# Performance work log

Measured on AMD Instinct MI355X. Metric: run time of the kernel, lower is better.

The kernel has to match this reference:

```python
import jax, jax.numpy as jnp
import numpy as np

N_HEADS = 8
KEY_DIM = 16
VALUE_DIM = 16
EMBED = N_HEADS * KEY_DIM  # 128
B, N = 32, 16384


def setup_inputs() -> dict:
    key = jax.random.key(0)
    k1, k2, k3, k4 = jax.random.split(key, 4)
    query = jax.random.normal(k1, (B, 1, EMBED), dtype=jnp.float32)
    keys = jax.random.normal(k2, (B, 1, N, EMBED), dtype=jnp.float32)
    values = jax.random.normal(k3, (B, 1, N, EMBED), dtype=jnp.float32)
    mask = jnp.zeros((B, 1, N), dtype=jnp.float32)  # additive mask
    W_out = jax.random.normal(k4, (N_HEADS * VALUE_DIM, EMBED), dtype=jnp.float32) * 0.05
    return {"query": query, "keys": keys, "values": values, "mask": mask, "W_out": W_out}


def _make_heads(v, d):
    # [B, N, H*d] -> [H, B, N, d]
    b, n, _ = v.shape
    return jnp.transpose(v.reshape(b, n, N_HEADS, d), (2, 0, 1, 3))


def reference(query, keys, values, mask, W_out):
    k = keys[:, 0]    # [B, N, E]
    v = values[:, 0]  # [B, N, E]
    q = _make_heads(query, KEY_DIM)   # [H, B, 1, dk]
    K = _make_heads(k, KEY_DIM)       # [H, B, N, dk]
    V = _make_heads(v, VALUE_DIM)     # [H, B, N, dv]
    scale = jnp.float32(KEY_DIM) ** 0.5
    attn = jnp.einsum('hbqd,hbnd->hbqn', q, K) / scale  # [H, B, 1, N]
    attn = attn + mask                                   # broadcast [B,1,N]
    attn = jax.nn.softmax(attn, axis=-1)
    heads = jnp.einsum('hbqn,hbnd->hbqd', attn, V)       # [H, B, 1, dv]
    b = heads.shape[1]
    concat = jnp.transpose(heads, (1, 2, 0, 3)).reshape(b, 1, N_HEADS * VALUE_DIM)
    return concat @ W_out  # [B, 1, E]
```

## Files before the change

kernel.cpp:

```cpp
#include <hip/hip_runtime.h>
#include <math.h>

#define NHEADS 8
#define KD 16
#define EMBED 128
#define BATCH 32
#define NSEQ 16384
#define NCHUNK 64
#define CHUNK (NSEQ / NCHUNK)
#define PART_STRIDE 18

typedef float f32x2 __attribute__((ext_vector_type(2)));

__global__ __launch_bounds__(256) void attn_partial(
    const float* __restrict__ q,
    const float* __restrict__ K,
    const float* __restrict__ V,
    const float* __restrict__ mask,
    float* __restrict__ part)
{
    const int b    = blockIdx.x >> 6;
    const int c    = blockIdx.x & 63;
    const int wave = threadIdx.x >> 6;
    const int lane = threadIdx.x & 63;
    const int head = lane >> 3;
    const int g    = lane & 7;

    const f32x2 q2 = *(const f32x2*)&q[b * EMBED + 2 * lane];

    float m = -INFINITY;
    float lsum = 0.f;
    float accx = 0.f, accy = 0.f;

    const size_t rowbase = (size_t)b * NSEQ;
    const int r0 = c * CHUNK;

    #pragma unroll 4
    for (int r = r0 + wave; r < r0 + CHUNK; r += 4) {
        const size_t off = (rowbase + r) * EMBED + 2 * lane;
        const f32x2 k2 = __builtin_nontemporal_load((const f32x2*)&K[off]);
        const f32x2 v2 = __builtin_nontemporal_load((const f32x2*)&V[off]);
        float p = q2.x * k2.x + q2.y * k2.y;
        p += __shfl_xor(p, 1);
        p += __shfl_xor(p, 2);
        p += __shfl_xor(p, 4);
        const float s  = p * 0.25f + mask[rowbase + r];
        const float mn = fmaxf(m, s);
        const float corr = __expf(m - mn);
        const float w    = __expf(s - mn);
        lsum = lsum * corr + w;
        accx = accx * corr + w * v2.x;
        accy = accy * corr + w * v2.y;
        m = mn;
    }

    __shared__ float lds[4][NHEADS][PART_STRIDE];
    lds[wave][head][2 + 2 * g]     = accx;
    lds[wave][head][2 + 2 * g + 1] = accy;
    if (g == 0) {
        lds[wave][head][0] = m;
        lds[wave][head][1] = lsum;
    }
    __syncthreads();

    const int t = threadIdx.x;
    if (t < EMBED) {
        const int h = t >> 4;
        const int d = t & 15;
        float M = -INFINITY;
        #pragma unroll
        for (int w = 0; w < 4; ++w) M = fmaxf(M, lds[w][h][0]);
        float L = 0.f, A = 0.f;
        #pragma unroll
        for (int w = 0; w < 4; ++w) {
            const float e = __expf(lds[w][h][0] - M);
            L += lds[w][h][1] * e;
            A += lds[w][h][2 + d] * e;
        }
        float* p = &part[((size_t)(b * NCHUNK + c) * NHEADS + h) * PART_STRIDE];
        p[2 + d] = A;
        if (d == 0) { p[0] = M; p[1] = L; }
    }
}

__global__ __launch_bounds__(128) void attn_finish(
    const float* __restrict__ part,
    const float* __restrict__ Wout,
    float* __restrict__ out)
{
    const int b = blockIdx.x;
    const int t = threadIdx.x;
    const int h = t >> 4;
    const int d = t & 15;

    __shared__ float heads[EMBED];

    float Mc[4], Lc[4], Ac[4];
    #pragma unroll
    for (int j = 0; j < 4; ++j) { Mc[j] = -INFINITY; Lc[j] = 0.f; Ac[j] = 0.f; }

    #pragma unroll 4
    for (int i = 0; i < 16; ++i) {
        #pragma unroll
        for (int j = 0; j < 4; ++j) {
            const int c = j * 16 + i;
            const float* p = &part[((size_t)(b * NCHUNK + c) * NHEADS + h) * PART_STRIDE];
            const float mc = p[0];
            const float lc = p[1];
            const float ac = p[2 + d];
            const float Mn = fmaxf(Mc[j], mc);
            const float eM = __expf(Mc[j] - Mn);
            const float ec = __expf(mc - Mn);
            Lc[j] = Lc[j] * eM + lc * ec;
            Ac[j] = Ac[j] * eM + ac * ec;
            Mc[j] = Mn;
        }
    }

    const float M = fmaxf(fmaxf(Mc[0], Mc[1]), fmaxf(Mc[2], Mc[3]));
    float L = 0.f, A = 0.f;
    #pragma unroll
    for (int j = 0; j < 4; ++j) {
        const float e = __expf(Mc[j] - M);
        L += Lc[j] * e;
        A += Ac[j] * e;
    }
    heads[t] = A / L;
    __syncthreads();

    float o = 0.f;
    #pragma unroll 8
    for (int dd = 0; dd < EMBED; ++dd)
        o += heads[dd] * Wout[dd * EMBED + t];
    out[b * EMBED + t] = o;
}

extern "C" void kernel_launch(void* const* d_in, const int* in_sizes, int n_in,
                              void* d_out, int out_size, void* d_ws, size_t ws_size,
                              hipStream_t stream) {
    const float* q    = (const float*)d_in[0];
    const float* K    = (const float*)d_in[1];
    const float* V    = (const float*)d_in[2];
    const float* mask = (const float*)d_in[3];
    const float* Wout = (const float*)d_in[4];
    float* out  = (float*)d_out;
    float* part = (float*)d_ws;

    attn_partial<<<BATCH * NCHUNK, 256, 0, stream>>>(q, K, V, mask, part);
    attn_finish<<<BATCH, 128, 0, stream>>>(part, Wout, out);
}
```

Measured before the change: 89.77 us.

## Fuse partial and finish kernels with last-block atomic counter reduction

Merges the two launches into one kernel. Each block writes its partial softmax state, then increments a per-batch atomic counter, and the last block for each batch does the cross-chunk merge and the output projection. This removes the second kernel launch and its dependency gap. In exchange it adds a memset launch to reset the counters, plus fences and an atomic per block.

```diff
diff --git a/kernel.cpp b/kernel.cpp
--- a/kernel.cpp
+++ b/kernel.cpp
@@ -9,15 +9,19 @@
 #define NCHUNK 64
 #define CHUNK (NSEQ / NCHUNK)
 #define PART_STRIDE 18
+#define PART_FLOATS (BATCH * NCHUNK * NHEADS * PART_STRIDE)
 
 typedef float f32x2 __attribute__((ext_vector_type(2)));
 
-__global__ __launch_bounds__(256) void attn_partial(
+__global__ __launch_bounds__(256) void attn_fused(
     const float* __restrict__ q,
     const float* __restrict__ K,
     const float* __restrict__ V,
     const float* __restrict__ mask,
-    float* __restrict__ part)
+    const float* __restrict__ Wout,
+    float* __restrict__ out,
+    float* __restrict__ part,
+    unsigned int* __restrict__ cnt)
 {
     const int b    = blockIdx.x >> 6;
     const int c    = blockIdx.x & 63;
@@ -55,6 +59,9 @@
     }
 
     __shared__ float lds[4][NHEADS][PART_STRIDE];
+    __shared__ float heads[EMBED];
+    __shared__ int last_flag;
+
     lds[wave][head][2 + 2 * g]     = accx;
     lds[wave][head][2 + 2 * g + 1] = accy;
     if (g == 0) {
@@ -81,58 +88,62 @@
         p[2 + d] = A;
         if (d == 0) { p[0] = M; p[1] = L; }
     }
-}
 
-__global__ __launch_bounds__(128) void attn_finish(
-    const float* __restrict__ part,
-    const float* __restrict__ Wout,
-    float* __restrict__ out)
-{
-    const int b = blockIdx.x;
-    const int t = threadIdx.x;
-    const int h = t >> 4;
-    const int d = t & 15;
+    __threadfence();
+    __syncthreads();
+    if (t == 0) {
+        const unsigned int old =
+            __hip_atomic_fetch_add(&cnt[b], 1u, __ATOMIC_ACQ_REL,
+                                   __HIP_MEMORY_SCOPE_AGENT);
+        last_flag = (old == NCHUNK - 1);
+    }
+    __syncthreads();
+    if (!last_flag) return;
 
-    __shared__ float heads[EMBED];
+    __threadfence();
 
-    float Mc[4], Lc[4], Ac[4];
-    #pragma unroll
-    for (int j = 0; j < 4; ++j) { Mc[j] = -INFINITY; Lc[j] = 0.f; Ac[j] = 0.f; }
-
-    #pragma unroll 4
-    for (int i = 0; i < 16; ++i) {
+    if (t < EMBED) {
+        const int h = t >> 4;
+        const int d = t & 15;
+        float Mc[4], Lc[4], Ac[4];
+        #pragma unroll
+        for (int j = 0; j < 4; ++j) { Mc[j] = -INFINITY; Lc[j] = 0.f; Ac[j] = 0.f; }
+        #pragma unroll 4
+        for (int i = 0; i < 16; ++i) {
+            #pragma unroll
+            for (int j = 0; j < 4; ++j) {
+                const int cc = j * 16 + i;
+                const float* p = &part[((size_t)(b * NCHUNK + cc) * NHEADS + h) * PART_STRIDE];
+                const float mc = p[0];
+                const float lc = p[1];
+                const float ac = p[2 + d];
+                const float Mn = fmaxf(Mc[j], mc);
+                const float eM = __expf(Mc[j] - Mn);
+                const float ec = __expf(mc - Mn);
+                Lc[j] = Lc[j] * eM + lc * ec;
+                Ac[j] = Ac[j] * eM + ac * ec;
+                Mc[j] = Mn;
+            }
+        }
+        const float M = fmaxf(fmaxf(Mc[0], Mc[1]), fmaxf(Mc[2], Mc[3]));
+        float L = 0.f, A = 0.f;
         #pragma unroll
         for (int j = 0; j < 4; ++j) {
-            const int c = j * 16 + i;
-            const float* p = &part[((size_t)(b * NCHUNK + c) * NHEADS + h) * PART_STRIDE];
-            const float mc = p[0];
-            const float lc = p[1];
-            const float ac = p[2 + d];
-            const float Mn = fmaxf(Mc[j], mc);
-            const float eM = __expf(Mc[j] - Mn);
-            const float ec = __expf(mc - Mn);
-            Lc[j] = Lc[j] * eM + lc * ec;
-            Ac[j] = Ac[j] * eM + ac * ec;
-            Mc[j] = Mn;
+            const float e = __expf(Mc[j] - M);
+            L += Lc[j] * e;
+            A += Ac[j] * e;
         }
+        heads[t] = A / L;
     }
-
-    const float M = fmaxf(fmaxf(Mc[0], Mc[1]), fmaxf(Mc[2], Mc[3]));
-    float L = 0.f, A = 0.f;
-    #pragma unroll
-    for (int j = 0; j < 4; ++j) {
-        const float e = __expf(Mc[j] - M);
-        L += Lc[j] * e;
-        A += Ac[j] * e;
-    }
-    heads[t] = A / L;
     __syncthreads();
 
-    float o = 0.f;
-    #pragma unroll 8
-    for (int dd = 0; dd < EMBED; ++dd)
-        o += heads[dd] * Wout[dd * EMBED + t];
-    out[b * EMBED + t] = o;
+    if (t < EMBED) {
+        float o = 0.f;
+        #pragma unroll 8
+        for (int dd = 0; dd < EMBED; ++dd)
+            o += heads[dd] * Wout[dd * EMBED + t];
+        out[b * EMBED + t] = o;
+    }
 }
 
 extern "C" void kernel_launch(void* const* d_in, const int* in_sizes, int n_in,
@@ -145,7 +156,9 @@
     const float* Wout = (const float*)d_in[4];
     float* out  = (float*)d_out;
     float* part = (float*)d_ws;
+    unsigned int* cnt = (unsigned int*)(part + PART_FLOATS);
 
-    attn_partial<<<BATCH * NCHUNK, 256, 0, stream>>>(q, K, V, mask, part);
-    attn_finish<<<BATCH, 128, 0, stream>>>(part, Wout, out);
+    hipMemsetAsync(cnt, 0, BATCH * sizeof(unsigned int), stream);
+    attn_fused<<<BATCH * NCHUNK, 256, 0, stream>>>(q, K, V, mask, Wout,
+                                                   out, part, cnt);
 }
```

Measured after the change: 316.6 us. 253% more time.
